# Kernel tuning notes

Hardware: AMD Instinct MI355X
Metric: run time of the kernel (lower is better)

Reference implementation:

```python
import jax, jax.numpy as jnp
import numpy as np

B_, T_, L_, M_, H_, F_ = 16, 2048, 128, 256, 512, 1024
EPS = 1e-5


def _init_reservoir(h, rng):
    # orthogonal matrix scaled inside the unit disk for a stable linear recurrence
    q, _ = np.linalg.qr(rng.standard_normal((h, h)).astype(np.float32))
    return jnp.asarray(0.95 * q, dtype=jnp.float32)


def setup_inputs() -> dict:
    key = jax.random.key(0)
    ks = jax.random.split(key, 8)
    rng = np.random.default_rng(0)
    s = lambda fan_in: 1.0 / np.sqrt(fan_in)
    return {
        "x": jax.random.normal(ks[0], (B_, T_, L_), dtype=jnp.float32),
        "We": jax.random.uniform(ks[1], (L_, M_), jnp.float32, -s(L_), s(L_)),
        "be": jnp.zeros((M_,), jnp.float32),
        "Wb": jax.random.uniform(ks[2], (M_, H_), jnp.float32, -s(M_), s(M_)),
        "A": _init_reservoir(H_, rng),
        "Wr": jax.random.uniform(ks[3], (L_, H_), jnp.float32, -s(L_), s(L_)),
        "br": jnp.zeros((H_,), jnp.float32),
        "ln_g": jnp.ones((H_,), jnp.float32),
        "ln_b": jnp.zeros((H_,), jnp.float32),
        "W1": jax.random.uniform(ks[4], (H_, F_), jnp.float32, -s(H_), s(H_)),
        "b1": jnp.zeros((F_,), jnp.float32),
        "W2": jax.random.uniform(ks[5], (F_, H_), jnp.float32, -s(F_), s(F_)),
        "b2": jnp.zeros((H_,), jnp.float32),
    }


def reference(x, We, be, Wb, A, Wr, br, ln_g, ln_b, W1, b1, W2, b2):
    # encoder + B projection, batched over all timesteps: [B,T,H]
    Bu = (x @ We + be) @ Wb

    # sequential linear recurrence h_t = h_{t-1} @ A + Bu_t, h_0 = Bu_0
    def step(h, bu_t):
        h = h @ A + bu_t
        return h, h

    h0 = jnp.zeros((x.shape[0], A.shape[0]), x.dtype)
    _, Hs = jax.lax.scan(step, h0, jnp.swapaxes(Bu, 0, 1))  # [T,B,H]
    H_seq = jnp.swapaxes(Hs, 0, 1)  # [B,T,H]

    # residual + layer norm
    z = H_seq + (x @ Wr + br)
    mu = jnp.mean(z, axis=-1, keepdims=True)
    var = jnp.mean(jnp.square(z - mu), axis=-1, keepdims=True)
    zn = (z - mu) * jax.lax.rsqrt(var + EPS) * ln_g + ln_b

    # MLP on last timestep
    h_last = zn[:, -1, :]
    out = jax.nn.relu(h_last @ W1 + b1) @ W2 + b2
    return out
```

## Files before the change

### kernel.cpp

```cpp
#include <hip/hip_runtime.h>

#define B_  16
#define T_  2048
#define L_  128
#define M_  256
#define H_  512
#define F_  1024
#define EPS 1e-5f

#define LDA_S 36
#define LDB_S 68
#define SMSZ (64 * LDA_S + 64 * LDB_S)

__device__ __forceinline__ float4 load_a4(const float* __restrict__ A,
                                          const float* __restrict__ Alast,
                                          int M, int lda, int amode,
                                          int gr, int gk) {
    float4 av = make_float4(0.f, 0.f, 0.f, 0.f);
    if (gr < M) {
        const float* p;
        if (amode == 1)
            p = A + (long)((gr & 15) * T_ + (T_ - 1 - (gr >> 4))) * L_ + gk;
        else if (amode == 2)
            p = A + (long)(((gr >> 4) << 5) + 16 + (gr & 15)) * lda + gk;
        else if (amode == 3 && gr == M - 1)
            p = Alast + gk;
        else
            p = A + (long)gr * lda + gk;
        av = *(const float4*)p;
    }
    return av;
}

__device__ __forceinline__ void gemm_tile(
    float* sm,
    const float* __restrict__ A, const float* __restrict__ Alast,
    const float* __restrict__ Bm, const float* __restrict__ bias,
    const float* __restrict__ Add, float* __restrict__ C,
    int M, int K, int lda, int ldb, int ldc,
    int flags, int amode, int bx, int by)
{
    constexpr int BM = 32, BN = 64, BK = 64, TM = 2, TN = 4;
    float* As = sm;
    float* Bs = sm + BK * LDA_S;
    const int tid = threadIdx.x;
    const int tx = tid & 15;
    const int ty = tid >> 4;
    const int row0 = by * BM, col0 = bx * BN;

    float4 pa[2], pb[4];
#pragma unroll
    for (int t = 0; t < 2; ++t) {
        int f = tid + t * 256;
        pa[t] = load_a4(A, Alast, M, lda, amode, row0 + (f >> 4), (f & 15) * 4);
    }
#pragma unroll
    for (int t = 0; t < 4; ++t) {
        int f = tid + t * 256;
        pb[t] = *(const float4*)(Bm + (long)(f >> 4) * ldb + col0 + (f & 15) * 4);
    }

    float acc[TM][TN] = {};

    for (int k0 = 0; k0 < K; k0 += BK) {
        __syncthreads();
#pragma unroll
        for (int t = 0; t < 2; ++t) {
            int f = tid + t * 256;
            int arow = f >> 4, kk = (f & 15) * 4;
            As[(kk + 0) * LDA_S + arow] = pa[t].x;
            As[(kk + 1) * LDA_S + arow] = pa[t].y;
            As[(kk + 2) * LDA_S + arow] = pa[t].z;
            As[(kk + 3) * LDA_S + arow] = pa[t].w;
        }
#pragma unroll
        for (int t = 0; t < 4; ++t) {
            int f = tid + t * 256;
            *(float4*)&Bs[(f >> 4) * LDB_S + (f & 15) * 4] = pb[t];
        }
        __syncthreads();
        int kn = k0 + BK;
        if (kn < K) {
#pragma unroll
            for (int t = 0; t < 2; ++t) {
                int f = tid + t * 256;
                pa[t] = load_a4(A, Alast, M, lda, amode, row0 + (f >> 4), kn + (f & 15) * 4);
            }
#pragma unroll
            for (int t = 0; t < 4; ++t) {
                int f = tid + t * 256;
                pb[t] = *(const float4*)(Bm + (long)(kn + (f >> 4)) * ldb + col0 + (f & 15) * 4);
            }
        }
#pragma unroll
        for (int kk = 0; kk < BK; ++kk) {
            float ra[TM], rb[TN];
#pragma unroll
            for (int i = 0; i < TM; ++i) ra[i] = As[kk * LDA_S + ty * TM + i];
#pragma unroll
            for (int j = 0; j < TN; ++j) rb[j] = Bs[kk * LDB_S + tx * TN + j];
#pragma unroll
            for (int i = 0; i < TM; ++i)
#pragma unroll
                for (int j = 0; j < TN; ++j)
                    acc[i][j] = fmaf(ra[i], rb[j], acc[i][j]);
        }
    }

#pragma unroll
    for (int i = 0; i < TM; ++i) {
        int r = row0 + ty * TM + i;
        if (r >= M) continue;
#pragma unroll
        for (int j = 0; j < TN; ++j) {
            int c = col0 + tx * TN + j;
            float v = acc[i][j];
            if (flags & 1) v += bias[c];
            if (amode == 2) v += Add[(long)(((r >> 4) << 5) + (r & 15)) * ldc + c];
            C[(long)r * ldc + c] = v;
        }
    }
}

__global__ __launch_bounds__(256) void dual(
    const float* A, const float* Alast, const float* Bm, const float* bias,
    const float* Add, float* C, int M, int K, int lda, int ldb, int ldc,
    int flags, int amode, int nbxA, int nA,
    const float* SqL, const float* SqR, float* SqOut)
{
    __shared__ float sm[SMSZ];
    int j = blockIdx.x;
    if (j < nA)
        gemm_tile(sm, A, Alast, Bm, bias, Add, C, M, K, lda, ldb, ldc,
                  flags, amode, j % nbxA, j / nbxA);
    else {
        int s = j - nA;
        gemm_tile(sm, SqL, nullptr, SqR, nullptr, nullptr, SqOut,
                  H_, H_, H_, H_, H_, 0, 0, s % 8, s / 8);
    }
}

#define TLDA 20
#define TLDB 68
#define TSM (64 * TLDA + 64 * TLDB)

template <int MODE>
__device__ __forceinline__ float4 tail_a4(const float* __restrict__ Asrc,
                                          const float* __restrict__ x,
                                          int b, int gk) {
    if (MODE == 0) {
        int seg = gk >> 9;
        if (seg < 3)
            return *(const float4*)(Asrc + (long)((seg + 1) * 16 + b) * H_ + (gk & 511));
        return *(const float4*)(x + ((long)b * T_ + (T_ - 1)) * L_ + (gk - 1536));
    } else if (MODE == 1) {
        return *(const float4*)(Asrc + (long)b * H_ + gk);
    } else {
        return *(const float4*)(Asrc + (long)b * F_ + gk);
    }
}

template <int MODE>
__device__ __forceinline__ float4 tail_b4(const float* __restrict__ P32,
                                          const float* __restrict__ P64,
                                          const float* __restrict__ P96,
                                          const float* __restrict__ WrB,
                                          int kr, int c) {
    if (MODE == 0) {
        const float* p;
        if (kr < 512)       p = P32 + (long)kr * H_;
        else if (kr < 1024) p = P64 + (long)(kr - 512) * H_;
        else if (kr < 1536) p = P96 + (long)(kr - 1024) * H_;
        else                p = WrB + (long)(kr - 1536) * H_;
        return *(const float4*)(p + c);
    } else if (MODE == 1) {
        return *(const float4*)(WrB + (long)kr * F_ + c);
    } else {
        return *(const float4*)(WrB + (long)kr * H_ + c);
    }
}

template <int MODE>
__global__ __launch_bounds__(256) void tailgemm(
    const float* __restrict__ Asrc, const float* __restrict__ x,
    const float* __restrict__ P32, const float* __restrict__ P64,
    const float* __restrict__ P96, const float* __restrict__ WrB,
    float* __restrict__ parts, int nbx, int kLen)
{
    constexpr int LDC = (MODE == 1) ? F_ : H_;
    __shared__ float sm[TSM];
    float* As = sm;
    float* Bs = sm + 64 * TLDA;
    const int tid = threadIdx.x;
    const int tx = tid & 15, ty = tid >> 4;
    const int kc = blockIdx.x / nbx;
    const int col0 = (blockIdx.x % nbx) * 64;
    const int kOff = kc * kLen;

    float4 pa, pb[4];
    {
        int gk = kOff + (tid & 15) * 4;
        pa = tail_a4<MODE>(Asrc, x, tid >> 4, gk);
#pragma unroll
        for (int t = 0; t < 4; ++t) {
            int f = tid + t * 256;
            pb[t] = tail_b4<MODE>(P32, P64, P96, WrB, kOff + (f >> 4), col0 + (f & 15) * 4);
        }
    }

    float acc[4] = {};
    for (int k0 = kOff; k0 < kOff + kLen; k0 += 64) {
        __syncthreads();
        {
            int arow = tid >> 4, kk = (tid & 15) * 4;
            As[(kk + 0) * TLDA + arow] = pa.x;
            As[(kk + 1) * TLDA + arow] = pa.y;
            As[(kk + 2) * TLDA + arow] = pa.z;
            As[(kk + 3) * TLDA + arow] = pa.w;
        }
#pragma unroll
        for (int t = 0; t < 4; ++t) {
            int f = tid + t * 256;
            *(float4*)&Bs[(f >> 4) * TLDB + (f & 15) * 4] = pb[t];
        }
        __syncthreads();
        int kn = k0 + 64;
        if (kn < kOff + kLen) {
            pa = tail_a4<MODE>(Asrc, x, tid >> 4, kn + (tid & 15) * 4);
#pragma unroll
            for (int t = 0; t < 4; ++t) {
                int f = tid + t * 256;
                pb[t] = tail_b4<MODE>(P32, P64, P96, WrB, kn + (f >> 4), col0 + (f & 15) * 4);
            }
        }
#pragma unroll
        for (int kk = 0; kk < 64; ++kk) {
            float ra = As[kk * TLDA + ty];
            float4 rb = *(float4*)&Bs[kk * TLDB + tx * 4];
            acc[0] = fmaf(ra, rb.x, acc[0]);
            acc[1] = fmaf(ra, rb.y, acc[1]);
            acc[2] = fmaf(ra, rb.z, acc[2]);
            acc[3] = fmaf(ra, rb.w, acc[3]);
        }
    }

    float* dst = parts + (long)kc * 16 * LDC + (long)ty * LDC + col0 + tx * 4;
    *(float4*)dst = make_float4(acc[0], acc[1], acc[2], acc[3]);
}

__global__ __launch_bounds__(256) void zlnred(
    const float* __restrict__ V1, const float* __restrict__ zparts,
    const float* __restrict__ br, const float* __restrict__ lng,
    const float* __restrict__ lnb, float* __restrict__ zn)
{
    __shared__ float red1[4], red2[4];
    const int b = blockIdx.x, tid = threadIdx.x;
    float z[2];
#pragma unroll
    for (int jj = 0; jj < 2; ++jj) {
        int c = tid + jj * 256;
        float s = V1[(long)b * H_ + c] + br[c];
#pragma unroll
        for (int kc = 0; kc < 13; ++kc)
            s += zparts[(long)kc * 16 * H_ + (long)b * H_ + c];
        z[jj] = s;
    }
    float s1 = z[0] + z[1];
    float s2 = z[0] * z[0] + z[1] * z[1];
#pragma unroll
    for (int off = 32; off > 0; off >>= 1) {
        s1 += __shfl_down(s1, off, 64);
        s2 += __shfl_down(s2, off, 64);
    }
    int wid = tid >> 6, lane = tid & 63;
    if (lane == 0) { red1[wid] = s1; red2[wid] = s2; }
    __syncthreads();
    float S1 = red1[0] + red1[1] + red1[2] + red1[3];
    float S2 = red2[0] + red2[1] + red2[2] + red2[3];
    float mu  = S1 * (1.0f / H_);
    float var = S2 * (1.0f / H_) - mu * mu;
    float rs  = rsqrtf(var + EPS);
#pragma unroll
    for (int jj = 0; jj < 2; ++jj) {
        int c = tid + jj * 256;
        zn[(long)b * H_ + c] = (z[jj] - mu) * rs * lng[c] + lnb[c];
    }
}

__global__ __launch_bounds__(256) void hred(
    const float* __restrict__ h1p, const float* __restrict__ b1,
    float* __restrict__ hid)
{
    int b = blockIdx.x >> 2;
    int c = (blockIdx.x & 3) * 256 + threadIdx.x;
    float s = b1[c];
#pragma unroll
    for (int kc = 0; kc < 4; ++kc)
        s += h1p[(long)kc * 16 * F_ + (long)b * F_ + c];
    hid[(long)b * F_ + c] = fmaxf(s, 0.f);
}

__global__ __launch_bounds__(256) void ored(
    const float* __restrict__ op, const float* __restrict__ b2,
    float* __restrict__ out)
{
    int b = blockIdx.x >> 1;
    int c = (blockIdx.x & 1) * 256 + threadIdx.x;
    float s = b2[c];
#pragma unroll
    for (int kc = 0; kc < 8; ++kc)
        s += op[(long)kc * 16 * H_ + (long)b * H_ + c];
    out[(long)b * H_ + c] = s;
}

extern "C" void kernel_launch(void* const* d_in, const int* in_sizes, int n_in,
                              void* d_out, int out_size, void* d_ws, size_t ws_size,
                              hipStream_t stream) {
    const float* x    = (const float*)d_in[0];
    const float* We   = (const float*)d_in[1];
    const float* be   = (const float*)d_in[2];
    const float* Wb   = (const float*)d_in[3];
    const float* Amat = (const float*)d_in[4];
    const float* Wr   = (const float*)d_in[5];
    const float* br   = (const float*)d_in[6];
    const float* lng  = (const float*)d_in[7];
    const float* lnb  = (const float*)d_in[8];
    const float* W1   = (const float*)d_in[9];
    const float* b1   = (const float*)d_in[10];
    const float* W2   = (const float*)d_in[11];
    const float* b2   = (const float*)d_in[12];
    float* out = (float*)d_out;

    float* ws  = (float*)d_ws;
    float* Wc  = ws;
    float* V0  = Wc + 129 * H_;
    float* V1  = V0 + 2048 * H_;
    float* P2  = V1 + 1024 * H_;
    float* P4  = P2 + H_ * H_;
    float* P8  = P4 + H_ * H_;
    float* P16 = P8 + H_ * H_;
    float* P32 = P16 + H_ * H_;
    float* P64 = P32 + H_ * H_;
    float* P96 = P64 + H_ * H_;
    float* zn  = P96 + H_ * H_;
    float* hid = zn + B_ * H_;
    float* zp  = hid + B_ * F_;
    float* h1p = zp + 13 * B_ * H_;
    float* op  = h1p + 4 * B_ * F_;

    dual<<<168, 256, 0, stream>>>(We, be, Wb, nullptr, nullptr, Wc,
                                  129, M_, M_, H_, H_, 0, 3, 8, 40,
                                  Amat, Amat, P2);
    dual<<<640, 256, 0, stream>>>(x, nullptr, Wc, Wc + 128 * H_, nullptr, V0,
                                  2048, L_, L_, H_, H_, 1, 1, 8, 512,
                                  P2, P2, P4);
    dual<<<384, 256, 0, stream>>>(V0, nullptr, Amat, nullptr, V0, V1,
                                  1024, H_, H_, H_, H_, 0, 2, 8, 256,
                                  P4, P4, P8);
    dual<<<256, 256, 0, stream>>>(V1, nullptr, P2, nullptr, V1, V0,
                                  512, H_, H_, H_, H_, 0, 2, 8, 128,
                                  P8, P8, P16);
    dual<<<192, 256, 0, stream>>>(V0, nullptr, P4, nullptr, V0, V1,
                                  256, H_, H_, H_, H_, 0, 2, 8, 64,
                                  P16, P16, P32);
    dual<<<160, 256, 0, stream>>>(V1, nullptr, P8, nullptr, V1, V0,
                                  128, H_, H_, H_, H_, 0, 2, 8, 32,
                                  P32, P32, P64);
    dual<<<144, 256, 0, stream>>>(V0, nullptr, P16, nullptr, V0, V1,
                                  64, H_, H_, H_, H_, 0, 2, 8, 16,
                                  P32, P64, P96);
    tailgemm<0><<<104, 256, 0, stream>>>(V1, x, P32, P64, P96, Wr, zp, 8, 128);
    zlnred<<<16, 256, 0, stream>>>(V1, zp, br, lng, lnb, zn);
    tailgemm<1><<<64, 256, 0, stream>>>(zn, nullptr, nullptr, nullptr, nullptr,
                                        W1, h1p, 16, 128);
    hred<<<64, 256, 0, stream>>>(h1p, b1, hid);
    tailgemm<2><<<64, 256, 0, stream>>>(hid, nullptr, nullptr, nullptr, nullptr,
                                        W2, op, 8, 128);
    ored<<<32, 256, 0, stream>>>(op, b2, out);
}
```

Before: 284.7 us.

## Fuse all stages into one cooperative persistent kernel with grid syncs

Replaces the chain of separate kernel launches (dual gemms, tail gemms, reductions) with a single cooperative kernel that walks each stage's tiles in a grid-stride loop and separates stages with grid-wide barriers. It targets the launch and inter-kernel gap cost across roughly a dozen small dependent launches. It first tries 512 blocks, then 256, and falls back to the old multi-kernel path if cooperative launch fails. Grid-sync cost and the reduced occupancy from a fixed block count may offset the savings, especially in the tiny tail stages.

```diff
diff --git a/kernel.cpp b/kernel.cpp
--- a/kernel.cpp
+++ b/kernel.cpp
@@ -1,4 +1,7 @@
 #include <hip/hip_runtime.h>
+#include <hip/hip_cooperative_groups.h>
+
+namespace cg = cooperative_groups;
 
 #define B_  16
 #define T_  2048
@@ -181,20 +184,20 @@
 }
 
 template <int MODE>
-__global__ __launch_bounds__(256) void tailgemm(
+__device__ __forceinline__ void tail_job(
+    float* sm,
     const float* __restrict__ Asrc, const float* __restrict__ x,
     const float* __restrict__ P32, const float* __restrict__ P64,
     const float* __restrict__ P96, const float* __restrict__ WrB,
-    float* __restrict__ parts, int nbx, int kLen)
+    float* __restrict__ parts, int nbx, int kLen, int jb)
 {
     constexpr int LDC = (MODE == 1) ? F_ : H_;
-    __shared__ float sm[TSM];
     float* As = sm;
     float* Bs = sm + 64 * TLDA;
     const int tid = threadIdx.x;
     const int tx = tid & 15, ty = tid >> 4;
-    const int kc = blockIdx.x / nbx;
-    const int col0 = (blockIdx.x % nbx) * 64;
+    const int kc = jb / nbx;
+    const int col0 = (jb % nbx) * 64;
     const int kOff = kc * kLen;
 
     float4 pa, pb[4];
@@ -248,69 +251,242 @@
     *(float4*)dst = make_float4(acc[0], acc[1], acc[2], acc[3]);
 }
 
+template <int MODE>
+__global__ __launch_bounds__(256) void tailgemm(
+    const float* __restrict__ Asrc, const float* __restrict__ x,
+    const float* __restrict__ P32, const float* __restrict__ P64,
+    const float* __restrict__ P96, const float* __restrict__ WrB,
+    float* __restrict__ parts, int nbx, int kLen)
+{
+    __shared__ float sm[TSM];
+    tail_job<MODE>(sm, Asrc, x, P32, P64, P96, WrB, parts, nbx, kLen, blockIdx.x);
+}
+
+__device__ __forceinline__ void zln_job(
+    float* red, const float* __restrict__ V1, const float* __restrict__ zparts,
+    const float* __restrict__ br, const float* __restrict__ lng,
+    const float* __restrict__ lnb, float* __restrict__ zn, int b)
+{
+    const int tid = threadIdx.x;
+    float z[2];
+#pragma unroll
+    for (int jj = 0; jj < 2; ++jj) {
+        int c = tid + jj * 256;
+        float s = V1[(long)b * H_ + c] + br[c];
+#pragma unroll
+        for (int kc = 0; kc < 13; ++kc)
+            s += zparts[(long)kc * 16 * H_ + (long)b * H_ + c];
+        z[jj] = s;
+    }
+    float s1 = z[0] + z[1];
+    float s2 = z[0] * z[0] + z[1] * z[1];
+#pragma unroll
+    for (int off = 32; off > 0; off >>= 1) {
+        s1 += __shfl_down(s1, off, 64);
+        s2 += __shfl_down(s2, off, 64);
+    }
+    int wid = tid >> 6, lane = tid & 63;
+    __syncthreads();
+    if (lane == 0) { red[wid] = s1; red[4 + wid] = s2; }
+    __syncthreads();
+    float S1 = red[0] + red[1] + red[2] + red[3];
+    float S2 = red[4] + red[5] + red[6] + red[7];
+    float mu  = S1 * (1.0f / H_);
+    float var = S2 * (1.0f / H_) - mu * mu;
+    float rs  = rsqrtf(var + EPS);
+#pragma unroll
+    for (int jj = 0; jj < 2; ++jj) {
+        int c = tid + jj * 256;
+        zn[(long)b * H_ + c] = (z[jj] - mu) * rs * lng[c] + lnb[c];
+    }
+}
+
 __global__ __launch_bounds__(256) void zlnred(
     const float* __restrict__ V1, const float* __restrict__ zparts,
     const float* __restrict__ br, const float* __restrict__ lng,
     const float* __restrict__ lnb, float* __restrict__ zn)
 {
-    __shared__ float red1[4], red2[4];
-    const int b = blockIdx.x, tid = threadIdx.x;
-    float z[2];
-#pragma unroll
-    for (int jj = 0; jj < 2; ++jj) {
-        int c = tid + jj * 256;
-        float s = V1[(long)b * H_ + c] + br[c];
-#pragma unroll
-        for (int kc = 0; kc < 13; ++kc)
-            s += zparts[(long)kc * 16 * H_ + (long)b * H_ + c];
-        z[jj] = s;
-    }
-    float s1 = z[0] + z[1];
-    float s2 = z[0] * z[0] + z[1] * z[1];
-#pragma unroll
-    for (int off = 32; off > 0; off >>= 1) {
-        s1 += __shfl_down(s1, off, 64);
-        s2 += __shfl_down(s2, off, 64);
-    }
-    int wid = tid >> 6, lane = tid & 63;
-    if (lane == 0) { red1[wid] = s1; red2[wid] = s2; }
-    __syncthreads();
-    float S1 = red1[0] + red1[1] + red1[2] + red1[3];
-    float S2 = red2[0] + red2[1] + red2[2] + red2[3];
-    float mu  = S1 * (1.0f / H_);
-    float var = S2 * (1.0f / H_) - mu * mu;
-    float rs  = rsqrtf(var + EPS);
-#pragma unroll
-    for (int jj = 0; jj < 2; ++jj) {
-        int c = tid + jj * 256;
-        zn[(long)b * H_ + c] = (z[jj] - mu) * rs * lng[c] + lnb[c];
-    }
+    __shared__ float red[8];
+    zln_job(red, V1, zparts, br, lng, lnb, zn, blockIdx.x);
+}
+
+__device__ __forceinline__ void hred_job(const float* __restrict__ h1p,
+                                         const float* __restrict__ b1,
+                                         float* __restrict__ hid, int j)
+{
+    int b = j >> 2;
+    int c = (j & 3) * 256 + threadIdx.x;
+    float s = b1[c];
+#pragma unroll
+    for (int kc = 0; kc < 4; ++kc)
+        s += h1p[(long)kc * 16 * F_ + (long)b * F_ + c];
+    hid[(long)b * F_ + c] = fmaxf(s, 0.f);
 }
 
 __global__ __launch_bounds__(256) void hred(
     const float* __restrict__ h1p, const float* __restrict__ b1,
     float* __restrict__ hid)
 {
-    int b = blockIdx.x >> 2;
-    int c = (blockIdx.x & 3) * 256 + threadIdx.x;
-    float s = b1[c];
-#pragma unroll
-    for (int kc = 0; kc < 4; ++kc)
-        s += h1p[(long)kc * 16 * F_ + (long)b * F_ + c];
-    hid[(long)b * F_ + c] = fmaxf(s, 0.f);
+    hred_job(h1p, b1, hid, blockIdx.x);
+}
+
+__device__ __forceinline__ void ored_job(const float* __restrict__ op,
+                                         const float* __restrict__ b2,
+                                         float* __restrict__ out, int j)
+{
+    int b = j >> 1;
+    int c = (j & 1) * 256 + threadIdx.x;
+    float s = b2[c];
+#pragma unroll
+    for (int kc = 0; kc < 8; ++kc)
+        s += op[(long)kc * 16 * H_ + (long)b * H_ + c];
+    out[(long)b * H_ + c] = s;
 }
 
 __global__ __launch_bounds__(256) void ored(
     const float* __restrict__ op, const float* __restrict__ b2,
     float* __restrict__ out)
 {
-    int b = blockIdx.x >> 1;
-    int c = (blockIdx.x & 1) * 256 + threadIdx.x;
-    float s = b2[c];
-#pragma unroll
-    for (int kc = 0; kc < 8; ++kc)
-        s += op[(long)kc * 16 * H_ + (long)b * H_ + c];
-    out[(long)b * H_ + c] = s;
+    ored_job(op, b2, out, blockIdx.x);
+}
+
+__global__ __launch_bounds__(256, 2) void mega(
+    const float* __restrict__ x, const float* __restrict__ We,
+    const float* __restrict__ be, const float* __restrict__ Wb,
+    const float* __restrict__ Amat, const float* __restrict__ Wr,
+    const float* __restrict__ br, const float* __restrict__ lng,
+    const float* __restrict__ lnb, const float* __restrict__ W1,
+    const float* __restrict__ b1, const float* __restrict__ W2,
+    const float* __restrict__ b2, float* __restrict__ out,
+    float* __restrict__ ws)
+{
+    __shared__ float sm[SMSZ];
+    float* Wc  = ws;
+    float* V0  = Wc + 129 * H_;
+    float* V1  = V0 + 2048 * H_;
+    float* P2  = V1 + 1024 * H_;
+    float* P4  = P2 + H_ * H_;
+    float* P8  = P4 + H_ * H_;
+    float* P16 = P8 + H_ * H_;
+    float* P32 = P16 + H_ * H_;
+    float* P64 = P32 + H_ * H_;
+    float* P96 = P64 + H_ * H_;
+    float* zn  = P96 + H_ * H_;
+    float* hid = zn + B_ * H_;
+    float* zp  = hid + B_ * F_;
+    float* h1p = zp + 13 * B_ * H_;
+    float* op  = h1p + 4 * B_ * F_;
+
+    cg::grid_group gg = cg::this_grid();
+    const int bid = blockIdx.x;
+    const int NB  = gridDim.x;
+
+    for (int j = bid; j < 168; j += NB) {
+        if (j < 40)
+            gemm_tile(sm, We, be, Wb, nullptr, nullptr, Wc,
+                      129, M_, M_, H_, H_, 0, 3, j & 7, j >> 3);
+        else {
+            int s = j - 40;
+            gemm_tile(sm, Amat, nullptr, Amat, nullptr, nullptr, P2,
+                      H_, H_, H_, H_, H_, 0, 0, s & 7, s >> 3);
+        }
+    }
+    gg.sync();
+
+    for (int j = bid; j < 640; j += NB) {
+        if (j < 512)
+            gemm_tile(sm, x, nullptr, Wc, Wc + 128 * H_, nullptr, V0,
+                      2048, L_, L_, H_, H_, 1, 1, j & 7, j >> 3);
+        else {
+            int s = j - 512;
+            gemm_tile(sm, P2, nullptr, P2, nullptr, nullptr, P4,
+                      H_, H_, H_, H_, H_, 0, 0, s & 7, s >> 3);
+        }
+    }
+    gg.sync();
+
+    for (int j = bid; j < 384; j += NB) {
+        if (j < 256)
+            gemm_tile(sm, V0, nullptr, Amat, nullptr, V0, V1,
+                      1024, H_, H_, H_, H_, 0, 2, j & 7, j >> 3);
+        else {
+            int s = j - 256;
+            gemm_tile(sm, P4, nullptr, P4, nullptr, nullptr, P8,
+                      H_, H_, H_, H_, H_, 0, 0, s & 7, s >> 3);
+        }
+    }
+    gg.sync();
+
+    for (int j = bid; j < 256; j += NB) {
+        if (j < 128)
+            gemm_tile(sm, V1, nullptr, P2, nullptr, V1, V0,
+                      512, H_, H_, H_, H_, 0, 2, j & 7, j >> 3);
+        else {
+            int s = j - 128;
+            gemm_tile(sm, P8, nullptr, P8, nullptr, nullptr, P16,
+                      H_, H_, H_, H_, H_, 0, 0, s & 7, s >> 3);
+        }
+    }
+    gg.sync();
+
+    for (int j = bid; j < 192; j += NB) {
+        if (j < 64)
+            gemm_tile(sm, V0, nullptr, P4, nullptr, V0, V1,
+                      256, H_, H_, H_, H_, 0, 2, j & 7, j >> 3);
+        else {
+            int s = j - 64;
+            gemm_tile(sm, P16, nullptr, P16, nullptr, nullptr, P32,
+                      H_, H_, H_, H_, H_, 0, 0, s & 7, s >> 3);
+        }
+    }
+    gg.sync();
+
+    for (int j = bid; j < 160; j += NB) {
+        if (j < 32)
+            gemm_tile(sm, V1, nullptr, P8, nullptr, V1, V0,
+                      128, H_, H_, H_, H_, 0, 2, j & 7, j >> 3);
+        else {
+            int s = j - 32;
+            gemm_tile(sm, P32, nullptr, P32, nullptr, nullptr, P64,
+                      H_, H_, H_, H_, H_, 0, 0, s & 7, s >> 3);
+        }
+    }
+    gg.sync();
+
+    for (int j = bid; j < 144; j += NB) {
+        if (j < 16)
+            gemm_tile(sm, V0, nullptr, P16, nullptr, V0, V1,
+                      64, H_, H_, H_, H_, 0, 2, j & 7, j >> 3);
+        else {
+            int s = j - 16;
+            gemm_tile(sm, P32, nullptr, P64, nullptr, nullptr, P96,
+                      H_, H_, H_, H_, H_, 0, 0, s & 7, s >> 3);
+        }
+    }
+    gg.sync();
+
+    for (int j = bid; j < 104; j += NB)
+        tail_job<0>(sm, V1, x, P32, P64, P96, Wr, zp, 8, 128, j);
+    gg.sync();
+
+    for (int j = bid; j < 16; j += NB)
+        zln_job(sm, V1, zp, br, lng, lnb, zn, j);
+    gg.sync();
+
+    for (int j = bid; j < 64; j += NB)
+        tail_job<1>(sm, zn, nullptr, nullptr, nullptr, nullptr, W1, h1p, 16, 128, j);
+    gg.sync();
+
+    for (int j = bid; j < 64; j += NB)
+        hred_job(h1p, b1, hid, j);
+    gg.sync();
+
+    for (int j = bid; j < 64; j += NB)
+        tail_job<2>(sm, hid, nullptr, nullptr, nullptr, nullptr, W2, op, 8, 128, j);
+    gg.sync();
+
+    for (int j = bid; j < 32; j += NB)
+        ored_job(op, b2, out, j);
 }
 
 extern "C" void kernel_launch(void* const* d_in, const int* in_sizes, int n_in,
@@ -330,8 +506,23 @@
     const float* W2   = (const float*)d_in[11];
     const float* b2   = (const float*)d_in[12];
     float* out = (float*)d_out;
-
     float* ws  = (float*)d_ws;
+
+    void* kargs[] = {
+        (void*)&x,   (void*)&We,  (void*)&be,  (void*)&Wb,  (void*)&Amat,
+        (void*)&Wr,  (void*)&br,  (void*)&lng, (void*)&lnb, (void*)&W1,
+        (void*)&b1,  (void*)&W2,  (void*)&b2,  (void*)&out, (void*)&ws };
+
+    hipError_t e = hipLaunchCooperativeKernel((const void*)mega, dim3(512),
+                                              dim3(256), kargs, 0, stream);
+    if (e != hipSuccess) {
+        (void)hipGetLastError();
+        e = hipLaunchCooperativeKernel((const void*)mega, dim3(256),
+                                       dim3(256), kargs, 0, stream);
+    }
+    if (e == hipSuccess) return;
+    (void)hipGetLastError();
+
     float* Wc  = ws;
     float* V0  = Wc + 129 * H_;
     float* V1  = V0 + 2048 * H_;
```

Measured after the change: 961.2 us. 3.38x slower.

## Fuse layernorm into first MLP GEMM and drop split-K reductions in tail

Applied to the files above, without the earlier changes.

The tail stage drops from six launches to three. Layernorm is recomputed per block inside the W1 GEMM, and the MLP GEMMs run full-K without split-K partials, so the hred and ored reduction kernels go away. This removes launch overhead and partial-buffer round trips. In exchange the two MLP GEMMs now run on only 16 and 8 blocks with long serial K loops, which gives much less parallelism and may lengthen each kernel.

```diff
diff --git a/kernel.cpp b/kernel.cpp
--- a/kernel.cpp
+++ b/kernel.cpp
@@ -144,72 +144,53 @@
 #define TLDB 68
 #define TSM (64 * TLDA + 64 * TLDB)
 
-template <int MODE>
-__device__ __forceinline__ float4 tail_a4(const float* __restrict__ Asrc,
-                                          const float* __restrict__ x,
-                                          int b, int gk) {
-    if (MODE == 0) {
-        int seg = gk >> 9;
-        if (seg < 3)
-            return *(const float4*)(Asrc + (long)((seg + 1) * 16 + b) * H_ + (gk & 511));
-        return *(const float4*)(x + ((long)b * T_ + (T_ - 1)) * L_ + (gk - 1536));
-    } else if (MODE == 1) {
-        return *(const float4*)(Asrc + (long)b * H_ + gk);
-    } else {
-        return *(const float4*)(Asrc + (long)b * F_ + gk);
-    }
-}
-
-template <int MODE>
-__device__ __forceinline__ float4 tail_b4(const float* __restrict__ P32,
-                                          const float* __restrict__ P64,
-                                          const float* __restrict__ P96,
-                                          const float* __restrict__ WrB,
-                                          int kr, int c) {
-    if (MODE == 0) {
-        const float* p;
-        if (kr < 512)       p = P32 + (long)kr * H_;
-        else if (kr < 1024) p = P64 + (long)(kr - 512) * H_;
-        else if (kr < 1536) p = P96 + (long)(kr - 1024) * H_;
-        else                p = WrB + (long)(kr - 1536) * H_;
-        return *(const float4*)(p + c);
-    } else if (MODE == 1) {
-        return *(const float4*)(WrB + (long)kr * F_ + c);
-    } else {
-        return *(const float4*)(WrB + (long)kr * H_ + c);
-    }
-}
-
-template <int MODE>
-__global__ __launch_bounds__(256) void tailgemm(
-    const float* __restrict__ Asrc, const float* __restrict__ x,
+__device__ __forceinline__ float4 z_a4(const float* __restrict__ V1,
+                                       const float* __restrict__ x,
+                                       int b, int gk) {
+    int seg = gk >> 9;
+    if (seg < 3)
+        return *(const float4*)(V1 + (long)((seg + 1) * 16 + b) * H_ + (gk & 511));
+    return *(const float4*)(x + ((long)b * T_ + (T_ - 1)) * L_ + (gk - 1536));
+}
+
+__device__ __forceinline__ float4 z_b4(const float* __restrict__ P32,
+                                       const float* __restrict__ P64,
+                                       const float* __restrict__ P96,
+                                       const float* __restrict__ Wr,
+                                       int kr, int c) {
+    const float* p;
+    if (kr < 512)       p = P32 + (long)kr * H_;
+    else if (kr < 1024) p = P64 + (long)(kr - 512) * H_;
+    else if (kr < 1536) p = P96 + (long)(kr - 1024) * H_;
+    else                p = Wr + (long)(kr - 1536) * H_;
+    return *(const float4*)(p + c);
+}
+
+__global__ __launch_bounds__(256) void zpart(
+    const float* __restrict__ V1, const float* __restrict__ x,
     const float* __restrict__ P32, const float* __restrict__ P64,
-    const float* __restrict__ P96, const float* __restrict__ WrB,
-    float* __restrict__ parts, int nbx, int kLen)
+    const float* __restrict__ P96, const float* __restrict__ Wr,
+    float* __restrict__ zp)
 {
-    constexpr int LDC = (MODE == 1) ? F_ : H_;
     __shared__ float sm[TSM];
     float* As = sm;
     float* Bs = sm + 64 * TLDA;
     const int tid = threadIdx.x;
     const int tx = tid & 15, ty = tid >> 4;
-    const int kc = blockIdx.x / nbx;
-    const int col0 = (blockIdx.x % nbx) * 64;
-    const int kOff = kc * kLen;
+    const int kc = blockIdx.x >> 3;
+    const int col0 = (blockIdx.x & 7) * 64;
+    const int kOff = kc * 128;
 
     float4 pa, pb[4];
-    {
-        int gk = kOff + (tid & 15) * 4;
-        pa = tail_a4<MODE>(Asrc, x, tid >> 4, gk);
-#pragma unroll
-        for (int t = 0; t < 4; ++t) {
-            int f = tid + t * 256;
-            pb[t] = tail_b4<MODE>(P32, P64, P96, WrB, kOff + (f >> 4), col0 + (f & 15) * 4);
-        }
+    pa = z_a4(V1, x, tid >> 4, kOff + (tid & 15) * 4);
+#pragma unroll
+    for (int t = 0; t < 4; ++t) {
+        int f = tid + t * 256;
+        pb[t] = z_b4(P32, P64, P96, Wr, kOff + (f >> 4), col0 + (f & 15) * 4);
     }
 
     float acc[4] = {};
-    for (int k0 = kOff; k0 < kOff + kLen; k0 += 64) {
+    for (int k0 = kOff; k0 < kOff + 128; k0 += 64) {
         __syncthreads();
         {
             int arow = tid >> 4, kk = (tid & 15) * 4;
@@ -225,12 +206,12 @@
         }
         __syncthreads();
         int kn = k0 + 64;
-        if (kn < kOff + kLen) {
-            pa = tail_a4<MODE>(Asrc, x, tid >> 4, kn + (tid & 15) * 4);
+        if (kn < kOff + 128) {
+            pa = z_a4(V1, x, tid >> 4, kn + (tid & 15) * 4);
 #pragma unroll
             for (int t = 0; t < 4; ++t) {
                 int f = tid + t * 256;
-                pb[t] = tail_b4<MODE>(P32, P64, P96, WrB, kn + (f >> 4), col0 + (f & 15) * 4);
+                pb[t] = z_b4(P32, P64, P96, Wr, kn + (f >> 4), col0 + (f & 15) * 4);
             }
         }
 #pragma unroll
@@ -244,73 +225,170 @@
         }
     }
 
-    float* dst = parts + (long)kc * 16 * LDC + (long)ty * LDC + col0 + tx * 4;
+    float* dst = zp + (long)kc * 16 * H_ + (long)ty * H_ + col0 + tx * 4;
     *(float4*)dst = make_float4(acc[0], acc[1], acc[2], acc[3]);
 }
 
-__global__ __launch_bounds__(256) void zlnred(
-    const float* __restrict__ V1, const float* __restrict__ zparts,
+__global__ __launch_bounds__(256) void mlp1z(
+    const float* __restrict__ V1, const float* __restrict__ zp,
     const float* __restrict__ br, const float* __restrict__ lng,
-    const float* __restrict__ lnb, float* __restrict__ zn)
+    const float* __restrict__ lnb, const float* __restrict__ W1,
+    const float* __restrict__ b1, float* __restrict__ hid)
 {
-    __shared__ float red1[4], red2[4];
-    const int b = blockIdx.x, tid = threadIdx.x;
-    float z[2];
-#pragma unroll
-    for (int jj = 0; jj < 2; ++jj) {
-        int c = tid + jj * 256;
-        float s = V1[(long)b * H_ + c] + br[c];
-#pragma unroll
-        for (int kc = 0; kc < 13; ++kc)
-            s += zparts[(long)kc * 16 * H_ + (long)b * H_ + c];
-        z[jj] = s;
-    }
-    float s1 = z[0] + z[1];
-    float s2 = z[0] * z[0] + z[1] * z[1];
-#pragma unroll
-    for (int off = 32; off > 0; off >>= 1) {
-        s1 += __shfl_down(s1, off, 64);
-        s2 += __shfl_down(s2, off, 64);
-    }
-    int wid = tid >> 6, lane = tid & 63;
-    if (lane == 0) { red1[wid] = s1; red2[wid] = s2; }
+    __shared__ float znL[16 * 512];
+    __shared__ float Bs[64 * TLDB];
+    const int tid = threadIdx.x;
+
+    {
+        const int r = tid >> 4;
+        const int l = tid & 15;
+        float4 zv[8];
+        float s1 = 0.f, s2 = 0.f;
+#pragma unroll
+        for (int i = 0; i < 8; ++i) {
+            int c = l * 4 + i * 64;
+            float4 v = *(const float4*)(V1 + (long)r * H_ + c);
+            float4 bb = *(const float4*)(br + c);
+            v.x += bb.x; v.y += bb.y; v.z += bb.z; v.w += bb.w;
+#pragma unroll
+            for (int kc = 0; kc < 13; ++kc) {
+                float4 p = *(const float4*)(zp + (long)kc * 16 * H_ + (long)r * H_ + c);
+                v.x += p.x; v.y += p.y; v.z += p.z; v.w += p.w;
+            }
+            zv[i] = v;
+            s1 += v.x + v.y + v.z + v.w;
+            s2 += v.x * v.x + v.y * v.y + v.z * v.z + v.w * v.w;
+        }
+#pragma unroll
+        for (int off = 1; off < 16; off <<= 1) {
+            s1 += __shfl_xor(s1, off, 64);
+            s2 += __shfl_xor(s2, off, 64);
+        }
+        float mu  = s1 * (1.0f / H_);
+        float var = s2 * (1.0f / H_) - mu * mu;
+        float rs  = rsqrtf(var + EPS);
+#pragma unroll
+        for (int i = 0; i < 8; ++i) {
+            int c = l * 4 + i * 64;
+            float4 g  = *(const float4*)(lng + c);
+            float4 bt = *(const float4*)(lnb + c);
+            float4 v  = zv[i];
+            v.x = (v.x - mu) * rs * g.x + bt.x;
+            v.y = (v.y - mu) * rs * g.y + bt.y;
+            v.z = (v.z - mu) * rs * g.z + bt.z;
+            v.w = (v.w - mu) * rs * g.w + bt.w;
+            *(float4*)&znL[r * 512 + c] = v;
+        }
+    }
     __syncthreads();
-    float S1 = red1[0] + red1[1] + red1[2] + red1[3];
-    float S2 = red2[0] + red2[1] + red2[2] + red2[3];
-    float mu  = S1 * (1.0f / H_);
-    float var = S2 * (1.0f / H_) - mu * mu;
-    float rs  = rsqrtf(var + EPS);
-#pragma unroll
-    for (int jj = 0; jj < 2; ++jj) {
-        int c = tid + jj * 256;
-        zn[(long)b * H_ + c] = (z[jj] - mu) * rs * lng[c] + lnb[c];
-    }
-}
-
-__global__ __launch_bounds__(256) void hred(
-    const float* __restrict__ h1p, const float* __restrict__ b1,
-    float* __restrict__ hid)
+
+    const int tx = tid & 15, ty = tid >> 4;
+    const int col0 = blockIdx.x * 64;
+
+    float4 pb[4];
+#pragma unroll
+    for (int t = 0; t < 4; ++t) {
+        int f = tid + t * 256;
+        pb[t] = *(const float4*)(W1 + (long)(f >> 4) * F_ + col0 + (f & 15) * 4);
+    }
+    float acc[4] = {};
+    for (int k0 = 0; k0 < H_; k0 += 64) {
+        __syncthreads();
+#pragma unroll
+        for (int t = 0; t < 4; ++t) {
+            int f = tid + t * 256;
+            *(float4*)&Bs[(f >> 4) * TLDB + (f & 15) * 4] = pb[t];
+        }
+        __syncthreads();
+        int kn = k0 + 64;
+        if (kn < H_) {
+#pragma unroll
+            for (int t = 0; t < 4; ++t) {
+                int f = tid + t * 256;
+                pb[t] = *(const float4*)(W1 + (long)(kn + (f >> 4)) * F_ + col0 + (f & 15) * 4);
+            }
+        }
+#pragma unroll
+        for (int kk = 0; kk < 64; ++kk) {
+            float ra = znL[ty * 512 + k0 + kk];
+            float4 rb = *(float4*)&Bs[kk * TLDB + tx * 4];
+            acc[0] = fmaf(ra, rb.x, acc[0]);
+            acc[1] = fmaf(ra, rb.y, acc[1]);
+            acc[2] = fmaf(ra, rb.z, acc[2]);
+            acc[3] = fmaf(ra, rb.w, acc[3]);
+        }
+    }
+    int c = col0 + tx * 4;
+    float4 v;
+    v.x = fmaxf(acc[0] + b1[c + 0], 0.f);
+    v.y = fmaxf(acc[1] + b1[c + 1], 0.f);
+    v.z = fmaxf(acc[2] + b1[c + 2], 0.f);
+    v.w = fmaxf(acc[3] + b1[c + 3], 0.f);
+    *(float4*)(hid + (long)ty * F_ + c) = v;
+}
+
+__global__ __launch_bounds__(256) void mlp2k(
+    const float* __restrict__ hid, const float* __restrict__ W2,
+    const float* __restrict__ b2, float* __restrict__ out)
 {
-    int b = blockIdx.x >> 2;
-    int c = (blockIdx.x & 3) * 256 + threadIdx.x;
-    float s = b1[c];
-#pragma unroll
-    for (int kc = 0; kc < 4; ++kc)
-        s += h1p[(long)kc * 16 * F_ + (long)b * F_ + c];
-    hid[(long)b * F_ + c] = fmaxf(s, 0.f);
-}
-
-__global__ __launch_bounds__(256) void ored(
-    const float* __restrict__ op, const float* __restrict__ b2,
-    float* __restrict__ out)
-{
-    int b = blockIdx.x >> 1;
-    int c = (blockIdx.x & 1) * 256 + threadIdx.x;
-    float s = b2[c];
-#pragma unroll
-    for (int kc = 0; kc < 8; ++kc)
-        s += op[(long)kc * 16 * H_ + (long)b * H_ + c];
-    out[(long)b * H_ + c] = s;
+    __shared__ float sm[TSM];
+    float* As = sm;
+    float* Bs = sm + 64 * TLDA;
+    const int tid = threadIdx.x;
+    const int tx = tid & 15, ty = tid >> 4;
+    const int col0 = blockIdx.x * 64;
+
+    float4 pa, pb[4];
+    pa = *(const float4*)(hid + (long)(tid >> 4) * F_ + (tid & 15) * 4);
+#pragma unroll
+    for (int t = 0; t < 4; ++t) {
+        int f = tid + t * 256;
+        pb[t] = *(const float4*)(W2 + (long)(f >> 4) * H_ + col0 + (f & 15) * 4);
+    }
+
+    float acc[4] = {};
+    for (int k0 = 0; k0 < F_; k0 += 64) {
+        __syncthreads();
+        {
+            int arow = tid >> 4, kk = (tid & 15) * 4;
+            As[(kk + 0) * TLDA + arow] = pa.x;
+            As[(kk + 1) * TLDA + arow] = pa.y;
+            As[(kk + 2) * TLDA + arow] = pa.z;
+            As[(kk + 3) * TLDA + arow] = pa.w;
+        }
+#pragma unroll
+        for (int t = 0; t < 4; ++t) {
+            int f = tid + t * 256;
+            *(float4*)&Bs[(f >> 4) * TLDB + (f & 15) * 4] = pb[t];
+        }
+        __syncthreads();
+        int kn = k0 + 64;
+        if (kn < F_) {
+            pa = *(const float4*)(hid + (long)(tid >> 4) * F_ + kn + (tid & 15) * 4);
+#pragma unroll
+            for (int t = 0; t < 4; ++t) {
+                int f = tid + t * 256;
+                pb[t] = *(const float4*)(W2 + (long)(kn + (f >> 4)) * H_ + col0 + (f & 15) * 4);
+            }
+        }
+#pragma unroll
+        for (int kk = 0; kk < 64; ++kk) {
+            float ra = As[kk * TLDA + ty];
+            float4 rb = *(float4*)&Bs[kk * TLDB + tx * 4];
+            acc[0] = fmaf(ra, rb.x, acc[0]);
+            acc[1] = fmaf(ra, rb.y, acc[1]);
+            acc[2] = fmaf(ra, rb.z, acc[2]);
+            acc[3] = fmaf(ra, rb.w, acc[3]);
+        }
+    }
+
+    int c = col0 + tx * 4;
+    float4 v;
+    v.x = acc[0] + b2[c + 0];
+    v.y = acc[1] + b2[c + 1];
+    v.z = acc[2] + b2[c + 2];
+    v.w = acc[3] + b2[c + 3];
+    *(float4*)(out + (long)ty * H_ + c) = v;
 }
 
 extern "C" void kernel_launch(void* const* d_in, const int* in_sizes, int n_in,
@@ -342,11 +420,8 @@
     float* P32 = P16 + H_ * H_;
     float* P64 = P32 + H_ * H_;
     float* P96 = P64 + H_ * H_;
-    float* zn  = P96 + H_ * H_;
-    float* hid = zn + B_ * H_;
+    float* hid = P96 + H_ * H_;
     float* zp  = hid + B_ * F_;
-    float* h1p = zp + 13 * B_ * H_;
-    float* op  = h1p + 4 * B_ * F_;
 
     dual<<<168, 256, 0, stream>>>(We, be, Wb, nullptr, nullptr, Wc,
                                   129, M_, M_, H_, H_, 0, 3, 8, 40,
@@ -369,12 +444,7 @@
     dual<<<144, 256, 0, stream>>>(V0, nullptr, P16, nullptr, V0, V1,
                                   64, H_, H_, H_, H_, 0, 2, 8, 16,
                                   P32, P64, P96);
-    tailgemm<0><<<104, 256, 0, stream>>>(V1, x, P32, P64, P96, Wr, zp, 8, 128);
-    zlnred<<<16, 256, 0, stream>>>(V1, zp, br, lng, lnb, zn);
-    tailgemm<1><<<64, 256, 0, stream>>>(zn, nullptr, nullptr, nullptr, nullptr,
-                                        W1, h1p, 16, 128);
-    hred<<<64, 256, 0, stream>>>(h1p, b1, hid);
-    tailgemm<2><<<64, 256, 0, stream>>>(hid, nullptr, nullptr, nullptr, nullptr,
-                                        W2, op, 8, 128);
-    ored<<<32, 256, 0, stream>>>(op, b2, out);
-}
+    zpart<<<104, 256, 0, stream>>>(V1, x, P32, P64, P96, Wr, zp);
+    mlp1z<<<16, 256, 0, stream>>>(V1, zp, br, lng, lnb, W1, b1, hid);
+    mlp2k<<<8, 256, 0, stream>>>(hid, W2, b2, out);
+}
```

Result: slower. 326.9 us (+14.9%).
